# Kernel tuning notes

Hardware: AMD Instinct MI355X
Metric: run time of the kernel (lower is better)

## Reference

```python
import jax, jax.numpy as jnp
import numpy as np
import math

D_MODEL = 2048
N_HEADS = 16
D_HEAD = D_MODEL // N_HEADS  # 128, also the RoPE dim
ROPE_BASE = 10000.0
B, T = 2, 2048


def _rope_cos_sin(seq_len, dim, dtype):
    inv_freq = 1.0 / (ROPE_BASE ** (jnp.arange(0, dim, 2, dtype=jnp.float32) / dim))
    t = jnp.arange(seq_len, dtype=jnp.float32)
    freqs = jnp.einsum('i,j->ij', t, inv_freq)          # [T, dim/2]
    emb = jnp.concatenate((freqs, freqs), axis=-1)       # [T, dim]  (half-concat layout, as in source)
    cos = jnp.cos(emb)[None, None, :, :].astype(dtype)   # [1,1,T,dim]
    sin = jnp.sin(emb)[None, None, :, :].astype(dtype)
    return cos, sin


def _apply_rot(x, cos, sin, dim):
    # interleaved pair rotation, faithful to the torch code
    x1 = x[..., 0:dim:2]
    x2 = x[..., 1:dim:2]
    x_rot = jnp.stack((-x2, x1), axis=-1).reshape(x.shape[:-1] + (dim,))
    return x[..., :dim] * cos + x_rot * sin


def setup_inputs() -> dict:
    key = jax.random.key(0)
    k1, k2, k3 = jax.random.split(key, 3)
    x = jax.random.normal(k1, (B, T, D_MODEL), dtype=jnp.float32)
    # causal additive mask, broadcastable to [B,H,T,T]
    neg = jnp.finfo(jnp.float32).min / 2
    causal = jnp.triu(jnp.full((T, T), neg, dtype=jnp.float32), k=1)
    mask = causal[None, None, :, :]
    Wqkv = jax.random.normal(k2, (D_MODEL, 3 * D_MODEL), dtype=jnp.float32) * (1.0 / math.sqrt(D_MODEL))
    bqkv = jnp.zeros((3 * D_MODEL,), dtype=jnp.float32)
    Wo = jax.random.normal(k3, (D_MODEL, D_MODEL), dtype=jnp.float32) * (1.0 / math.sqrt(D_MODEL))
    bo = jnp.zeros((D_MODEL,), dtype=jnp.float32)
    return {"x": x, "mask": mask, "Wqkv": Wqkv, "bqkv": bqkv, "Wo": Wo, "bo": bo}


def reference(x, mask, Wqkv, bqkv, Wo, bo):
    Bx, Tx, C = x.shape
    qkv = x @ Wqkv + bqkv                                     # [B,T,3C]
    qkv = qkv.reshape(Bx, Tx, 3, N_HEADS, D_HEAD)
    qkv = jnp.transpose(qkv, (2, 0, 3, 1, 4))                 # [3,B,H,T,dh]
    q, k, v = qkv[0], qkv[1], qkv[2]
    cos, sin = _rope_cos_sin(Tx, D_HEAD, x.dtype)
    q = _apply_rot(q, cos, sin, D_HEAD)
    k = _apply_rot(k, cos, sin, D_HEAD)
    att = jnp.einsum('bhqd,bhkd->bhqk', q, k) / math.sqrt(D_HEAD)
    att = att + mask
    att = jax.nn.softmax(att, axis=-1)
    y = jnp.einsum('bhqk,bhkd->bhqd', att, v)                 # [B,H,T,dh]
    y = jnp.transpose(y, (0, 2, 1, 3)).reshape(Bx, Tx, C)
    return y @ Wo + bo
```

## Files before the change

### kernel.cpp

```cpp
#include <hip/hip_runtime.h>
#include <stdint.h>

#define TDIM 2048
#define DMODEL 2048
#define NHEADS 16
#define DHEAD 128
#define NBATCH 2
#define NTOK (NBATCH * TDIM)
#define NQKV (3 * DMODEL)
#define BHTOT (NBATCH * NHEADS)

typedef unsigned short u16;
typedef __attribute__((ext_vector_type(8))) short bf16x8;
typedef __attribute__((ext_vector_type(4))) float f32x4;
typedef __attribute__((ext_vector_type(4))) int i32x4;

__device__ __forceinline__ u16 f2bf(float f) {
  union { float f; uint32_t u; } v; v.f = f;
  uint32_t u = v.u + 0x7fffu + ((v.u >> 16) & 1u);
  return (u16)(u >> 16);
}
__device__ __forceinline__ float bf2f(u16 h) {
  union { uint32_t u; float f; } v; v.u = ((uint32_t)h) << 16;
  return v.f;
}

#define GLOAD16(g, l)                                                        \
  __builtin_amdgcn_global_load_lds(                                          \
      (const __attribute__((address_space(1))) void*)(g),                    \
      (__attribute__((address_space(3))) void*)(l), 16, 0, 0)

__global__ void rope_table_kernel(float* __restrict__ ct, float* __restrict__ st) {
  int idx = blockIdx.x * 256 + threadIdx.x;
  int t = idx >> 6, m = idx & 63;
  float inv = expf(-(float)m * (9.210340371976184f / 64.0f));
  float ang = (float)t * inv;
  ct[idx] = cosf(ang);
  st[idx] = sinf(ang);
}

__global__ void convert_kernel(const float* __restrict__ in, u16* __restrict__ out) {
  int i = blockIdx.x * 256 + threadIdx.x;
  float4 v = ((const float4*)in)[i];
  ushort4 o;
  o.x = f2bf(v.x); o.y = f2bf(v.y); o.z = f2bf(v.z); o.w = f2bf(v.w);
  ((ushort4*)out)[i] = o;
}

__global__ __launch_bounds__(256) void transpose_convert_kernel(
    const float* __restrict__ in, u16* __restrict__ out, int K, int N) {
  __shared__ u16 tile[32][33];
  int n0 = blockIdx.x * 32, k0 = blockIdx.y * 32;
  int tx = threadIdx.x, ty = threadIdx.y;
  #pragma unroll
  for (int q = 0; q < 4; q++) {
    int k = ty + q * 8;
    tile[k][tx] = f2bf(in[(size_t)(k0 + k) * N + n0 + tx]);
  }
  __syncthreads();
  #pragma unroll
  for (int q = 0; q < 4; q++) {
    int n = ty + q * 8;
    out[(size_t)(n0 + n) * K + k0 + tx] = tile[tx][n];
  }
}

__global__ __launch_bounds__(256) void vtrans_kernel(
    const u16* __restrict__ Vtmp, u16* __restrict__ Vt) {
  __shared__ u16 tile[32][33];
  int bh = blockIdx.z;
  int t0 = blockIdx.x * 32, d0 = blockIdx.y * 32;
  int tx = threadIdx.x, ty = threadIdx.y;
  const u16* src = Vtmp + (size_t)bh * TDIM * DHEAD;
  u16* dst = Vt + (size_t)bh * DHEAD * TDIM;
  #pragma unroll
  for (int q = 0; q < 4; q++) {
    int t = ty + q * 8;
    tile[t][tx] = src[(size_t)(t0 + t) * DHEAD + d0 + tx];
  }
  __syncthreads();
  #pragma unroll
  for (int q = 0; q < 4; q++) {
    int d = ty + q * 8;
    dst[(size_t)(d0 + d) * TDIM + t0 + tx] = tile[tx][d];
  }
}

template <int MODE>
__global__ __launch_bounds__(512, 2) void gemm_bt_kernel(
    const u16* __restrict__ A, const u16* __restrict__ Bt,
    const float* __restrict__ bias,
    u16* __restrict__ q_out, u16* __restrict__ k_out, u16* __restrict__ v_out,
    float* __restrict__ f_out,
    const float* __restrict__ ct, const float* __restrict__ st, int K) {
  __shared__ __attribute__((aligned(128))) char lds[3][49152];
  const int tid = threadIdx.x;
  const int lane = tid & 63, w = tid >> 6;
  const int wr = w >> 2, wc = w & 3;
  const int g = lane >> 4, c = lane & 15;
  const int m0 = blockIdx.x * 128, n0 = blockIdx.y * 256;
  const size_t rowb = (size_t)K * 2;
  const int NKT = K >> 6;

  const char* aSrc[2]; int aDst[2];
  const char* bSrc[4]; int bDst[4];
  #pragma unroll
  for (int p = 0; p < 2; p++) {
    int o = p * 8192 + tid * 16;
    int row = o >> 7, j = (o >> 4) & 7;
    aSrc[p] = (const char*)A + (size_t)(m0 + row) * rowb + ((j ^ (row & 7)) << 4);
    aDst[p] = o;
  }
  #pragma unroll
  for (int p = 0; p < 4; p++) {
    int o = p * 8192 + tid * 16;
    int row = o >> 7, j = (o >> 4) & 7;
    bSrc[p] = (const char*)Bt + (size_t)(n0 + row) * rowb + ((j ^ (row & 7)) << 4);
    bDst[p] = 16384 + o;
  }

#define STAGE(bufp, kt)                                                      \
  {                                                                          \
    const size_t kb_ = (size_t)(kt) * 128;                                   \
    _Pragma("unroll") for (int p_ = 0; p_ < 2; p_++)                         \
        GLOAD16(aSrc[p_] + kb_, (bufp) + aDst[p_]);                          \
    _Pragma("unroll") for (int p_ = 0; p_ < 4; p_++)                         \
        GLOAD16(bSrc[p_] + kb_, (bufp) + bDst[p_]);                          \
  }

  int aRd[4][2], bRd[4][2];
  #pragma unroll
  for (int m = 0; m < 4; m++) {
    #pragma unroll
    for (int ks = 0; ks < 2; ks++) {
      int arow = wr * 64 + m * 16 + c;
      aRd[m][ks] = arow * 128 + (((ks * 4 + g) ^ (c & 7)) << 4);
      int brow = wc * 64 + m * 16 + c;
      bRd[m][ks] = 16384 + brow * 128 + (((ks * 4 + g) ^ (c & 7)) << 4);
    }
  }

  const f32x4 zero = {0.f, 0.f, 0.f, 0.f};
  f32x4 acc[4][4];
  #pragma unroll
  for (int m = 0; m < 4; m++)
    #pragma unroll
    for (int n = 0; n < 4; n++) acc[m][n] = zero;

  STAGE(lds[0], 0);
  STAGE(lds[1], 1);

  for (int kt = 0; kt < NKT; kt++) {
    if (kt + 1 < NKT) {
      asm volatile("s_waitcnt vmcnt(6)" ::: "memory");
    } else {
      asm volatile("s_waitcnt vmcnt(0)" ::: "memory");
    }
    __builtin_amdgcn_s_barrier();
    __builtin_amdgcn_sched_barrier(0);

    char* bp = lds[kt % 3];
    if (kt + 2 < NKT) STAGE(lds[(kt + 2) % 3], kt + 2);

    bf16x8 afr[4][2], bfr[4][2];
    #pragma unroll
    for (int n = 0; n < 4; n++)
      #pragma unroll
      for (int ks = 0; ks < 2; ks++)
        bfr[n][ks] = *(const bf16x8*)(bp + bRd[n][ks]);
    #pragma unroll
    for (int m = 0; m < 4; m++)
      #pragma unroll
      for (int ks = 0; ks < 2; ks++)
        afr[m][ks] = *(const bf16x8*)(bp + aRd[m][ks]);

    __builtin_amdgcn_s_setprio(1);
    #pragma unroll
    for (int ks = 0; ks < 2; ks++)
      #pragma unroll
      for (int m = 0; m < 4; m++)
        #pragma unroll
        for (int n = 0; n < 4; n++)
          acc[m][n] = __builtin_amdgcn_mfma_f32_16x16x32_bf16(
              afr[m][ks], bfr[n][ks], acc[m][n], 0, 0, 0);
    __builtin_amdgcn_s_setprio(0);
    __builtin_amdgcn_sched_barrier(0);
  }
#undef STAGE

  #pragma unroll
  for (int m = 0; m < 4; m++) {
    #pragma unroll
    for (int n = 0; n < 4; n++) {
      int gcol = n0 + wc * 64 + n * 16 + c;
      float bv = bias[gcol];
      float val[4];
      #pragma unroll
      for (int r = 0; r < 4; r++) val[r] = acc[m][n][r] + bv;
      if (MODE == 0) {
        int s = n0 >> 11;
        int rem = gcol & 2047;
        int h = rem >> 7, d = rem & 127;
        int b0 = (m0 + wr * 64 + m * 16) >> 11;
        size_t hb = (((size_t)(b0 * NHEADS + h)) * TDIM) * DHEAD + d;
        if (s == 2) {
          #pragma unroll
          for (int r = 0; r < 4; r++) {
            int t = (m0 + wr * 64 + m * 16 + g * 4 + r) & (TDIM - 1);
            v_out[hb + (size_t)t * DHEAD] = f2bf(val[r]);
          }
        } else {
          int mf = gcol & 63;
          float sgn = (c & 1) ? 1.0f : -1.0f;
          u16* dst = (s == 0) ? q_out : k_out;
          float qs = (s == 0) ? 0.08838834764831845f : 1.0f;
          #pragma unroll
          for (int r = 0; r < 4; r++) {
            float part = __shfl_xor(val[r], 1, 64);
            int t = (m0 + wr * 64 + m * 16 + g * 4 + r) & (TDIM - 1);
            float cs = ct[t * 64 + mf], sn = st[t * 64 + mf];
            float rot = (val[r] * cs + sgn * part * sn) * qs;
            dst[hb + (size_t)t * DHEAD] = f2bf(rot);
          }
        }
      } else {
        #pragma unroll
        for (int r = 0; r < 4; r++) {
          int grow = m0 + wr * 64 + m * 16 + g * 4 + r;
          f_out[(size_t)grow * DMODEL + gcol] = val[r];
        }
      }
    }
  }
}

__global__ __launch_bounds__(256) void attn_kernel(
    const u16* __restrict__ Q, const u16* __restrict__ K,
    const u16* __restrict__ Vt, u16* __restrict__ Yattn) {
  __shared__ u16 Ks[2][64 * 128];
  __shared__ u16 Vs[2][128 * 64];
  __shared__ u16 Ps[4][16 * 64];
  const int tid = threadIdx.x, lane = tid & 63, w = tid >> 6;
  const int g = lane >> 4, c = lane & 15;
  const int bh = blockIdx.y, b = bh >> 4, h = bh & 15;
  const u16* Qp = Q + (size_t)bh * TDIM * DHEAD;
  const u16* Kp = K + (size_t)bh * TDIM * DHEAD;
  const u16* Vp = Vt + (size_t)bh * DHEAD * TDIM;
  const f32x4 zero = {0.f, 0.f, 0.f, 0.f};

  for (int half = 0; half < 2; half++) {
    const int qt = half ? (31 - (int)blockIdx.x) : (int)blockIdx.x;
    const int qb = qt * 64 + w * 16;

    bf16x8 qf[4];
    #pragma unroll
    for (int kc = 0; kc < 4; kc++)
      qf[kc] = *(const bf16x8*)(Qp + (size_t)(qb + c) * DHEAD + kc * 32 + g * 8);

    f32x4 po[8];
    #pragma unroll
    for (int df = 0; df < 8; df++) po[df] = zero;
    float mrun[4], lrun[4];
    #pragma unroll
    for (int r = 0; r < 4; r++) { mrun[r] = -1e30f; lrun[r] = 0.f; }

    const int nt = qt + 1;

    {
      #pragma unroll
      for (int p = 0; p < 4; p++) {
        int off = p * 4096 + tid * 16;
        int kr = off >> 8, kc4 = (off & 255) >> 4;
        GLOAD16((const char*)Kp + (size_t)kr * 256 + ((kc4 ^ (kr & 7)) << 4),
                (char*)Ks[0] + off);
        int vr = off >> 7, vc4 = (off & 127) >> 4;
        GLOAD16((const char*)Vp + (size_t)vr * (TDIM * 2) + ((vc4 ^ (vr & 7)) << 4),
                (char*)Vs[0] + off);
      }
    }
    __syncthreads();

    int cur = 0;
    for (int t = 0; t < nt; t++) {
      if (t + 1 < nt) {
        int kv0n = (t + 1) * 64;
        char* KsN = (char*)Ks[cur ^ 1];
        char* VsN = (char*)Vs[cur ^ 1];
        #pragma unroll
        for (int p = 0; p < 4; p++) {
          int off = p * 4096 + tid * 16;
          int kr = off >> 8, kc4 = (off & 255) >> 4;
          GLOAD16((const char*)Kp + (size_t)(kv0n + kr) * 256 +
                      ((kc4 ^ (kr & 7)) << 4),
                  KsN + off);
          int vr = off >> 7, vc4 = (off & 127) >> 4;
          GLOAD16((const char*)Vp + (size_t)vr * (TDIM * 2) + (size_t)kv0n * 2 +
                      ((vc4 ^ (vr & 7)) << 4),
                  VsN + off);
        }
      }

      const u16* KsC = Ks[cur];
      const u16* VsC = Vs[cur];
      const int kv0 = t * 64;

      f32x4 sa[4];
      #pragma unroll
      for (int n = 0; n < 4; n++) sa[n] = zero;
      __builtin_amdgcn_s_setprio(1);
      #pragma unroll
      for (int n = 0; n < 4; n++) {
        int krow = n * 16 + c;
        #pragma unroll
        for (int kc = 0; kc < 4; kc++) {
          int kb = (kc * 32 + g * 8) * 2;
          bf16x8 kf = *(const bf16x8*)((const char*)KsC + krow * 256 +
                                       (kb ^ ((krow & 7) << 4)));
          sa[n] = __builtin_amdgcn_mfma_f32_16x16x32_bf16(qf[kc], kf, sa[n], 0, 0, 0);
        }
      }
      __builtin_amdgcn_s_setprio(0);

      if (kv0 + 63 > qb) {
        #pragma unroll
        for (int n = 0; n < 4; n++) {
          int col = kv0 + n * 16 + c;
          #pragma unroll
          for (int r = 0; r < 4; r++) {
            int qrow = qb + g * 4 + r;
            if (col > qrow) sa[n][r] = -1e30f;
          }
        }
      }

      float pvals[4][4];
      #pragma unroll
      for (int r = 0; r < 4; r++) {
        float vmax = fmaxf(fmaxf(sa[0][r], sa[1][r]), fmaxf(sa[2][r], sa[3][r]));
        #pragma unroll
        for (int d = 1; d < 16; d <<= 1) vmax = fmaxf(vmax, __shfl_xor(vmax, d, 64));
        float mnew = fmaxf(mrun[r], vmax);
        float scale = __expf(mrun[r] - mnew);
        float rs = 0.f;
        #pragma unroll
        for (int n = 0; n < 4; n++) {
          float p = __expf(sa[n][r] - mnew);
          pvals[r][n] = p;
          rs += p;
        }
        #pragma unroll
        for (int d = 1; d < 16; d <<= 1) rs += __shfl_xor(rs, d, 64);
        lrun[r] = lrun[r] * scale + rs;
        mrun[r] = mnew;
        #pragma unroll
        for (int df = 0; df < 8; df++) po[df][r] *= scale;
      }

      char* Pw = (char*)&Ps[w][0];
      #pragma unroll
      for (int r = 0; r < 4; r++) {
        int ri = g * 4 + r;
        #pragma unroll
        for (int n = 0; n < 4; n++) {
          int colb = (n * 16 + c) * 2;
          *(u16*)(Pw + ri * 128 + (colb ^ ((ri & 7) << 4))) = f2bf(pvals[r][n]);
        }
      }
      bf16x8 pa[2];
      #pragma unroll
      for (int kc2 = 0; kc2 < 2; kc2++) {
        int pb = (kc2 * 32 + g * 8) * 2;
        pa[kc2] = *(const bf16x8*)(Pw + c * 128 + (pb ^ ((c & 7) << 4)));
      }
      __builtin_amdgcn_s_setprio(1);
      #pragma unroll
      for (int df = 0; df < 8; df++) {
        #pragma unroll
        for (int kc2 = 0; kc2 < 2; kc2++) {
          int vrow = df * 16 + c;
          int vb = (kc2 * 32 + g * 8) * 2;
          bf16x8 vf = *(const bf16x8*)((const char*)VsC + vrow * 128 +
                                       (vb ^ ((vrow & 7) << 4)));
          po[df] = __builtin_amdgcn_mfma_f32_16x16x32_bf16(pa[kc2], vf, po[df], 0, 0, 0);
        }
      }
      __builtin_amdgcn_s_setprio(0);

      __syncthreads();
      cur ^= 1;
    }

    float inv[4];
    #pragma unroll
    for (int r = 0; r < 4; r++) inv[r] = 1.0f / lrun[r];
    #pragma unroll
    for (int df = 0; df < 8; df++) {
      #pragma unroll
      for (int r = 0; r < 4; r++) {
        int trow = qb + g * 4 + r;
        int col = h * DHEAD + df * 16 + c;
        Yattn[((size_t)b * TDIM + trow) * DMODEL + col] = f2bf(po[df][r] * inv[r]);
      }
    }
  }
}

extern "C" void kernel_launch(void* const* d_in, const int* in_sizes, int n_in,
                              void* d_out, int out_size, void* d_ws, size_t ws_size,
                              hipStream_t stream) {
  const float* x    = (const float*)d_in[0];
  const float* Wqkv = (const float*)d_in[2];
  const float* bqkv = (const float*)d_in[3];
  const float* Wo   = (const float*)d_in[4];
  const float* bo   = (const float*)d_in[5];
  float* out = (float*)d_out;

  char* ws = (char*)d_ws;
  size_t o = 0;
  u16* xb    = (u16*)(ws + o); o += (size_t)NTOK * DMODEL * 2;
  u16* Wqkvt = (u16*)(ws + o); o += (size_t)NQKV * DMODEL * 2;
  u16* Wot   = (u16*)(ws + o); o += (size_t)DMODEL * DMODEL * 2;
  u16* Qb    = (u16*)(ws + o); o += (size_t)BHTOT * TDIM * DHEAD * 2;
  u16* Kb    = (u16*)(ws + o); o += (size_t)BHTOT * TDIM * DHEAD * 2;
  u16* Vtmp  = (u16*)(ws + o); o += (size_t)BHTOT * TDIM * DHEAD * 2;
  float* ct  = (float*)(ws + o); o += (size_t)TDIM * 64 * 4;
  float* st  = (float*)(ws + o); o += (size_t)TDIM * 64 * 4;
  u16* Vt    = xb;
  u16* Yattn = Vtmp;

  dim3 tb32x8(32, 8);

  rope_table_kernel<<<(TDIM * 64) / 256, 256, 0, stream>>>(ct, st);
  convert_kernel<<<(NTOK * DMODEL / 4) / 256, 256, 0, stream>>>(x, xb);
  transpose_convert_kernel<<<dim3(NQKV / 32, DMODEL / 32), tb32x8, 0, stream>>>(
      Wqkv, Wqkvt, DMODEL, NQKV);
  transpose_convert_kernel<<<dim3(DMODEL / 32, DMODEL / 32), tb32x8, 0, stream>>>(
      Wo, Wot, DMODEL, DMODEL);

  gemm_bt_kernel<0><<<dim3(NTOK / 128, NQKV / 256), 512, 0, stream>>>(
      xb, Wqkvt, bqkv, Qb, Kb, Vtmp, nullptr, ct, st, DMODEL);

  vtrans_kernel<<<dim3(TDIM / 32, DHEAD / 32, BHTOT), tb32x8, 0, stream>>>(Vtmp, Vt);

  attn_kernel<<<dim3(16, BHTOT), 256, 0, stream>>>(Qb, Kb, Vt, Yattn);

  gemm_bt_kernel<1><<<dim3(NTOK / 128, DMODEL / 256), 512, 0, stream>>>(
      Yattn, Wot, bo, nullptr, nullptr, nullptr, out, nullptr, nullptr, DMODEL);
}
```

Before: 294.1 us.

## Split GEMM k-tile into two half-phases interleaving LDS reads, staging and MFMA

Restructures the GEMM main loop so each 64-wide k-tile is processed in two 32-wide halves. Each half loads its own A/B fragments, issues half of the next global-to-LDS stage, then runs MFMAs between extra workgroup barriers. The aim is to spread global load issue and LDS reads across the tile and to cut fragment register pressure, in the style of a ping-pong schedule. In exchange it adds four barriers per k-tile, which may add synchronisation stalls.

```diff
diff --git a/kernel.cpp b/kernel.cpp
--- a/kernel.cpp
+++ b/kernel.cpp
@@ -102,30 +102,27 @@
   const size_t rowb = (size_t)K * 2;
   const int NKT = K >> 6;
 
-  const char* aSrc[2]; int aDst[2];
-  const char* bSrc[4]; int bDst[4];
+  const char* sSrc[6]; int sDst[6];
   #pragma unroll
   for (int p = 0; p < 2; p++) {
     int o = p * 8192 + tid * 16;
     int row = o >> 7, j = (o >> 4) & 7;
-    aSrc[p] = (const char*)A + (size_t)(m0 + row) * rowb + ((j ^ (row & 7)) << 4);
-    aDst[p] = o;
+    sSrc[p] = (const char*)A + (size_t)(m0 + row) * rowb + ((j ^ (row & 7)) << 4);
+    sDst[p] = o;
   }
   #pragma unroll
   for (int p = 0; p < 4; p++) {
     int o = p * 8192 + tid * 16;
     int row = o >> 7, j = (o >> 4) & 7;
-    bSrc[p] = (const char*)Bt + (size_t)(n0 + row) * rowb + ((j ^ (row & 7)) << 4);
-    bDst[p] = 16384 + o;
-  }
-
-#define STAGE(bufp, kt)                                                      \
+    sSrc[2 + p] = (const char*)Bt + (size_t)(n0 + row) * rowb + ((j ^ (row & 7)) << 4);
+    sDst[2 + p] = 16384 + o;
+  }
+
+#define STAGE3(bufp, kt, base)                                               \
   {                                                                          \
     const size_t kb_ = (size_t)(kt) * 128;                                   \
-    _Pragma("unroll") for (int p_ = 0; p_ < 2; p_++)                         \
-        GLOAD16(aSrc[p_] + kb_, (bufp) + aDst[p_]);                          \
-    _Pragma("unroll") for (int p_ = 0; p_ < 4; p_++)                         \
-        GLOAD16(bSrc[p_] + kb_, (bufp) + bDst[p_]);                          \
+    _Pragma("unroll") for (int p_ = 0; p_ < 3; p_++)                         \
+        GLOAD16(sSrc[(base) + p_] + kb_, (bufp) + sDst[(base) + p_]);        \
   }
 
   int aRd[4][2], bRd[4][2];
@@ -147,46 +144,67 @@
     #pragma unroll
     for (int n = 0; n < 4; n++) acc[m][n] = zero;
 
-  STAGE(lds[0], 0);
-  STAGE(lds[1], 1);
+  STAGE3(lds[0], 0, 0); STAGE3(lds[0], 0, 3);
+  STAGE3(lds[1], 1, 0); STAGE3(lds[1], 1, 3);
+  asm volatile("s_waitcnt vmcnt(6)" ::: "memory");
+  __builtin_amdgcn_s_barrier();
+  __builtin_amdgcn_sched_barrier(0);
 
   for (int kt = 0; kt < NKT; kt++) {
-    if (kt + 1 < NKT) {
-      asm volatile("s_waitcnt vmcnt(6)" ::: "memory");
-    } else {
-      asm volatile("s_waitcnt vmcnt(0)" ::: "memory");
-    }
-    __builtin_amdgcn_s_barrier();
-    __builtin_amdgcn_sched_barrier(0);
-
     char* bp = lds[kt % 3];
-    if (kt + 2 < NKT) STAGE(lds[(kt + 2) % 3], kt + 2);
-
-    bf16x8 afr[4][2], bfr[4][2];
-    #pragma unroll
-    for (int n = 0; n < 4; n++)
-      #pragma unroll
-      for (int ks = 0; ks < 2; ks++)
-        bfr[n][ks] = *(const bf16x8*)(bp + bRd[n][ks]);
-    #pragma unroll
-    for (int m = 0; m < 4; m++)
-      #pragma unroll
-      for (int ks = 0; ks < 2; ks++)
-        afr[m][ks] = *(const bf16x8*)(bp + aRd[m][ks]);
-
-    __builtin_amdgcn_s_setprio(1);
-    #pragma unroll
-    for (int ks = 0; ks < 2; ks++)
+    char* sp = lds[(kt + 2) % 3];
+    const bool do_stage = (kt + 2 < NKT);
+
+    {
+      bf16x8 afr[4], bfr[4];
+      #pragma unroll
+      for (int n = 0; n < 4; n++) bfr[n] = *(const bf16x8*)(bp + bRd[n][0]);
+      #pragma unroll
+      for (int m = 0; m < 4; m++) afr[m] = *(const bf16x8*)(bp + aRd[m][0]);
+      if (do_stage) STAGE3(sp, kt + 2, 0);
+      __builtin_amdgcn_s_barrier();
+      asm volatile("s_waitcnt lgkmcnt(0)" ::: "memory");
+      __builtin_amdgcn_sched_barrier(0);
+      __builtin_amdgcn_s_setprio(1);
       #pragma unroll
       for (int m = 0; m < 4; m++)
         #pragma unroll
         for (int n = 0; n < 4; n++)
           acc[m][n] = __builtin_amdgcn_mfma_f32_16x16x32_bf16(
-              afr[m][ks], bfr[n][ks], acc[m][n], 0, 0, 0);
-    __builtin_amdgcn_s_setprio(0);
-    __builtin_amdgcn_sched_barrier(0);
-  }
-#undef STAGE
+              afr[m], bfr[n], acc[m][n], 0, 0, 0);
+      __builtin_amdgcn_s_setprio(0);
+      __builtin_amdgcn_s_barrier();
+      __builtin_amdgcn_sched_barrier(0);
+    }
+
+    {
+      bf16x8 afr[4], bfr[4];
+      #pragma unroll
+      for (int n = 0; n < 4; n++) bfr[n] = *(const bf16x8*)(bp + bRd[n][1]);
+      #pragma unroll
+      for (int m = 0; m < 4; m++) afr[m] = *(const bf16x8*)(bp + aRd[m][1]);
+      if (do_stage) STAGE3(sp, kt + 2, 3);
+      if (do_stage) {
+        asm volatile("s_waitcnt vmcnt(6)" ::: "memory");
+      } else {
+        asm volatile("s_waitcnt vmcnt(0)" ::: "memory");
+      }
+      __builtin_amdgcn_s_barrier();
+      asm volatile("s_waitcnt lgkmcnt(0)" ::: "memory");
+      __builtin_amdgcn_sched_barrier(0);
+      __builtin_amdgcn_s_setprio(1);
+      #pragma unroll
+      for (int m = 0; m < 4; m++)
+        #pragma unroll
+        for (int n = 0; n < 4; n++)
+          acc[m][n] = __builtin_amdgcn_mfma_f32_16x16x32_bf16(
+              afr[m], bfr[n], acc[m][n], 0, 0, 0);
+      __builtin_amdgcn_s_setprio(0);
+      __builtin_amdgcn_s_barrier();
+      __builtin_amdgcn_sched_barrier(0);
+    }
+  }
+#undef STAGE3
 
   #pragma unroll
   for (int m = 0; m < 4; m++) {
```

Result: no change. 294.7 us (+0.2%).

## Double-buffer GEMM LDS with split-phase MFMA and swizzle workgroup order

Applied to the files above, without the earlier changes.

Cuts the GEMM's LDS from three stages to two. Each k-step is split into two halves: the second-half A fragments are read from LDS, a barrier is taken, and the next tile is staged into the same buffer while the second half of the MFMAs runs. This frees LDS, possibly allowing two blocks per CU, and keeps the prefetch depth. It also remaps the block index with a stride-8 swizzle to improve L2 reuse across neighbouring blocks. The cost is an extra barrier per iteration and tighter synchronisation that could expose global-load latency.

```diff
diff --git a/kernel.cpp b/kernel.cpp
--- a/kernel.cpp
+++ b/kernel.cpp
@@ -93,12 +93,18 @@
     u16* __restrict__ q_out, u16* __restrict__ k_out, u16* __restrict__ v_out,
     float* __restrict__ f_out,
     const float* __restrict__ ct, const float* __restrict__ st, int K) {
-  __shared__ __attribute__((aligned(128))) char lds[3][49152];
+  __shared__ __attribute__((aligned(128))) char lds[2][49152];
   const int tid = threadIdx.x;
   const int lane = tid & 63, w = tid >> 6;
   const int wr = w >> 2, wc = w & 3;
   const int g = lane >> 4, c = lane & 15;
-  const int m0 = blockIdx.x * 128, n0 = blockIdx.y * 256;
+
+  const int gx = gridDim.x;
+  const int nwg = gx * gridDim.y;
+  const int lin = (int)blockIdx.x + (int)blockIdx.y * gx;
+  const int swz = (lin & 7) * (nwg >> 3) + (lin >> 3);
+  const int m0 = (swz % gx) * 128, n0 = (swz / gx) * 256;
+
   const size_t rowb = (size_t)K * 2;
   const int NKT = K >> 6;
 
@@ -149,42 +155,63 @@
 
   STAGE(lds[0], 0);
   STAGE(lds[1], 1);
+  asm volatile("s_waitcnt vmcnt(6)" ::: "memory");
+  __builtin_amdgcn_s_barrier();
+  __builtin_amdgcn_sched_barrier(0);
 
   for (int kt = 0; kt < NKT; kt++) {
-    if (kt + 1 < NKT) {
-      asm volatile("s_waitcnt vmcnt(6)" ::: "memory");
-    } else {
-      asm volatile("s_waitcnt vmcnt(0)" ::: "memory");
-    }
-    __builtin_amdgcn_s_barrier();
-    __builtin_amdgcn_sched_barrier(0);
-
-    char* bp = lds[kt % 3];
-    if (kt + 2 < NKT) STAGE(lds[(kt + 2) % 3], kt + 2);
-
-    bf16x8 afr[4][2], bfr[4][2];
+    char* bp = lds[kt & 1];
+    bf16x8 bfr[4][2], afr[2][2], af2[2][2];
     #pragma unroll
     for (int n = 0; n < 4; n++)
       #pragma unroll
       for (int ks = 0; ks < 2; ks++)
         bfr[n][ks] = *(const bf16x8*)(bp + bRd[n][ks]);
     #pragma unroll
-    for (int m = 0; m < 4; m++)
+    for (int m = 0; m < 2; m++)
       #pragma unroll
       for (int ks = 0; ks < 2; ks++)
         afr[m][ks] = *(const bf16x8*)(bp + aRd[m][ks]);
-
     __builtin_amdgcn_s_setprio(1);
     #pragma unroll
     for (int ks = 0; ks < 2; ks++)
       #pragma unroll
-      for (int m = 0; m < 4; m++)
+      for (int m = 0; m < 2; m++)
         #pragma unroll
         for (int n = 0; n < 4; n++)
           acc[m][n] = __builtin_amdgcn_mfma_f32_16x16x32_bf16(
               afr[m][ks], bfr[n][ks], acc[m][n], 0, 0, 0);
     __builtin_amdgcn_s_setprio(0);
+
+    #pragma unroll
+    for (int m = 0; m < 2; m++)
+      #pragma unroll
+      for (int ks = 0; ks < 2; ks++)
+        af2[m][ks] = *(const bf16x8*)(bp + aRd[m + 2][ks]);
+    asm volatile("s_waitcnt lgkmcnt(0)" ::: "memory");
+    __builtin_amdgcn_s_barrier();
     __builtin_amdgcn_sched_barrier(0);
+    if (kt + 2 < NKT) STAGE(bp, kt + 2);
+    __builtin_amdgcn_s_setprio(1);
+    #pragma unroll
+    for (int ks = 0; ks < 2; ks++)
+      #pragma unroll
+      for (int m = 0; m < 2; m++)
+        #pragma unroll
+        for (int n = 0; n < 4; n++)
+          acc[m + 2][n] = __builtin_amdgcn_mfma_f32_16x16x32_bf16(
+              af2[m][ks], bfr[n][ks], acc[m + 2][n], 0, 0, 0);
+    __builtin_amdgcn_s_setprio(0);
+
+    if (kt < NKT - 1) {
+      if (kt + 2 < NKT) {
+        asm volatile("s_waitcnt vmcnt(6)" ::: "memory");
+      } else {
+        asm volatile("s_waitcnt vmcnt(0)" ::: "memory");
+      }
+      __builtin_amdgcn_s_barrier();
+      __builtin_amdgcn_sched_barrier(0);
+    }
   }
 #undef STAGE
 
```

New measurement: 298.1 us. About the same (+1.3%).
